# Kernel tuning notes

Measured on AMD Instinct MI355X. Metric: run time of the kernel, lower is better.

The kernel has to match this reference:

```python
import jax, jax.numpy as jnp
import numpy as np

N, E, C, L, G, O = 100000, 1600000, 128, 7, 2, 40
BETA = 0.9
HEADS, HC = 1, 128  # heads=1, head_channels=hidden_channels=128


def setup_inputs() -> dict:
    key = jax.random.key(0)
    ks = jax.random.split(key, 16)
    s = 0.05  # ~ torch Linear init std for fan_in=128
    inp = {
        'x': jax.random.normal(ks[0], (N, C), jnp.float32),
        'edge_index': jax.random.randint(ks[1], (2, E), 0, N, jnp.int64),
        'Wh': jax.random.normal(ks[2], (L, C, C)) * s,
        'bh': jax.random.normal(ks[3], (L, C)) * s,
        'Wg': jax.random.normal(ks[4], (L, C, C)) * s,
        'bg': jax.random.normal(ks[5], (L, C)) * s,
        'Wl': jax.random.normal(ks[6], (L, C, C)) * s,
        'bl': jax.random.normal(ks[7], (L, C)) * s,
        'ln_g': jnp.ones((L, C)), 'ln_b': jnp.zeros((L, C)),
        'bn_g': jnp.ones((L, C)), 'bn_b': jnp.zeros((L, C)),
        'bn_rm': jnp.zeros((L, C)), 'bn_rv': jnp.ones((L, C)),
        'gWh': jax.random.normal(ks[8], (G, C, C)) * s,
        'gbh': jax.random.normal(ks[9], (G, C)) * s,
        'gWk': jax.random.normal(ks[10], (G, C, C)) * s,
        'gWv': jax.random.normal(ks[11], (G, C, C)) * s,
        'gln_g': jnp.ones((G, C)), 'gln_b': jnp.zeros((G, C)),
        'gWo': jax.random.normal(ks[12], (G, C, C)) * s,
        'gbo': jax.random.normal(ks[13], (G, C)) * s,
        'f_ln_g': jnp.ones((C,)), 'f_ln_b': jnp.zeros((C,)),
        'Wp': jax.random.normal(ks[14], (O, C)) * s,
        'bp': jax.random.normal(ks[15], (O,)) * s,
    }
    return inp


def _layer_norm(x, g, b, eps=1e-5):
    mu = jnp.mean(x, axis=-1, keepdims=True)
    var = jnp.mean((x - mu) ** 2, axis=-1, keepdims=True)
    return (x - mu) * jax.lax.rsqrt(var + eps) * g + b


def reference(x, edge_index, Wh, bh, Wg, bg, Wl, bl, ln_g, ln_b,
              bn_g, bn_b, bn_rm, bn_rv, gWh, gbh, gWk, gWv,
              gln_g, gln_b, gWo, gbo, f_ln_g, f_ln_b, Wp, bp):
    n = x.shape[0]
    src, dst = edge_index[0], edge_index[1]
    # gcn_norm with add_self_loops=True: deg over destination incl. self loop
    deg = jnp.zeros((n,), x.dtype).at[dst].add(1.0) + 1.0
    dinv = jax.lax.rsqrt(deg)
    enorm = (dinv[src] * dinv[dst])[:, None]   # [E,1]
    selfw = (dinv * dinv)[:, None]             # [N,1] self-loop weight

    x_local = jnp.zeros_like(x @ Wh[0].T)
    for i in range(L):
        h = jax.nn.relu(x @ Wh[i].T + bh[i])
        xw = x @ Wg[i].T                                  # GCN lin (bias separate)
        agg = jax.ops.segment_sum(xw[src] * enorm, dst, num_segments=n)
        conv = agg + xw * selfw + bg[i]
        x = conv + x @ Wl[i].T + bl[i]
        # BatchNorm1d in eval mode (running stats)
        x = (x - bn_rm[i]) * jax.lax.rsqrt(bn_rv[i] + 1e-5) * bn_g[i] + bn_b[i]
        x = jax.nn.relu(x)
        x = (1.0 - BETA) * _layer_norm(h * x, ln_g[i], ln_b[i]) + BETA * x
        x_local = x_local + x

    # global linear attention (PolynormerAttention, qk_shared=True, qkv_bias=False)
    xg = _layer_norm(x_local, f_ln_g, f_ln_b)
    for j in range(G):
        h = xg @ gWh[j].T + gbh[j]
        k = jax.nn.sigmoid(xg @ gWk[j].T).reshape(n, HEADS, HC)
        q = k
        v = (xg @ gWv[j].T).reshape(n, HEADS, HC)
        kv = jnp.einsum('ndh,ndm->dhm', k, v)            # [heads,hc,hc]
        num = jnp.einsum('ndh,dhm->ndm', q, kv)          # [N,heads,hc]
        k_sum = jnp.sum(k, axis=0)                       # [heads,hc]
        den = jnp.einsum('ndh,dh->nd', q, k_sum)[..., None]
        attn = (num / (den + 1e-6)).reshape(n, HEADS * HC)
        xg = _layer_norm(attn, gln_g[j], gln_b[j]) * (h + BETA)
        xg = jax.nn.relu(xg @ gWo[j].T + gbo[j])

    return xg @ Wp.T + bp
```

## Files before the change

### kernel.cpp

```cpp
#include <hip/hip_runtime.h>

typedef unsigned short u16;
typedef unsigned int u32;
typedef __attribute__((ext_vector_type(8))) short short8;
typedef __attribute__((ext_vector_type(8))) unsigned short ushort8v;
typedef __attribute__((ext_vector_type(4))) float f32x4;

#define CDIM 128

__device__ __forceinline__ float b2f(u16 u){ return __uint_as_float(((unsigned)u)<<16); }
__device__ __forceinline__ u16 f2b(float f){
  unsigned x = __float_as_uint(f);
  unsigned r = (x + 0x7fffu + ((x>>16)&1u)) >> 16;
  return (u16)r;
}
__device__ __forceinline__ float wsum64(float v){
  #pragma unroll
  for(int d=1; d<64; d<<=1) v += __shfl_xor(v, d, 64);
  return v;
}
__device__ __forceinline__ float wsum16(float v){
  v += __shfl_xor(v, 1, 64);
  v += __shfl_xor(v, 2, 64);
  v += __shfl_xor(v, 4, 64);
  v += __shfl_xor(v, 8, 64);
  return v;
}

__global__ void k_probe(const u32* __restrict__ x, const u32* __restrict__ ei, int* __restrict__ flags){
  __shared__ int s_bf, s_nz;
  if(threadIdx.x == 0){ s_bf = 0; s_nz = 0; }
  __syncthreads();
  int c_bf = 0, c_nz = 0;
  for(int i = threadIdx.x; i < 4096; i += 256){
    u32 w = x[i];
    u32 e = (w >> 7) & 0xFFu;
    if(e >= 100u && e <= 140u) c_bf++;
    if(ei[2*i + 1] != 0u) c_nz++;
  }
  atomicAdd(&s_bf, c_bf);
  atomicAdd(&s_nz, c_nz);
  __syncthreads();
  if(threadIdx.x == 0){
    flags[0] = (s_bf < 2048) ? 1 : 0;
    flags[1] = (s_nz < 8) ? 1 : 0;
  }
}

__global__ void k_cvt_x(const void* __restrict__ src, u16* __restrict__ dst, int n,
                        const int* __restrict__ flags){
  int i = (blockIdx.x*256 + threadIdx.x)*8;
  if(i + 7 >= n) return;
  if(flags[0]){
    const float* s = (const float*)src + i;
    float4 a = *(const float4*)s;
    float4 b = *(const float4*)(s + 4);
    ushort8v o;
    o[0]=f2b(a.x); o[1]=f2b(a.y); o[2]=f2b(a.z); o[3]=f2b(a.w);
    o[4]=f2b(b.x); o[5]=f2b(b.y); o[6]=f2b(b.z); o[7]=f2b(b.w);
    *(ushort8v*)(dst + i) = o;
  } else {
    *(ushort8v*)(dst + i) = *(const ushort8v*)((const u16*)src + i);
  }
}

struct CvtArgs {
  const void* src[24];
  u16* dst[24];
  int n[24];
};

__global__ void k_cvt_params(CvtArgs a, const int* __restrict__ flags){
  int seg = blockIdx.y;
  int i = blockIdx.x*256 + threadIdx.x;
  int n = a.n[seg];
  if(i >= n) return;
  if(flags[0]) a.dst[seg][i] = f2b(((const float*)a.src[seg])[i]);
  else         a.dst[seg][i] = ((const u16*)a.src[seg])[i];
}

__global__ void k_cvt_ei_count(const int* __restrict__ src, int* __restrict__ dst, int E,
                               const int* __restrict__ flags, u32* __restrict__ cnt){
  int i = blockIdx.x*256 + threadIdx.x;
  if(i >= 2*E) return;
  int v = flags[1] ? src[2*i] : src[i];
  dst[i] = v;
  if(i >= E) atomicAdd(&cnt[v], 1u);
}

__global__ __launch_bounds__(256) void k_scan1(const u32* __restrict__ cnt, int n, u32* __restrict__ bsum){
  const int lane = threadIdx.x & 63;
  const int wv = threadIdx.x >> 6;
  int i = blockIdx.x*256 + threadIdx.x;
  u32 v = (i < n) ? cnt[i] : 0u;
  #pragma unroll
  for(int d=1; d<64; d<<=1) v += (u32)__shfl_xor((int)v, d, 64);
  __shared__ u32 ws[4];
  if(lane == 0) ws[wv] = v;
  __syncthreads();
  if(threadIdx.x == 0) bsum[blockIdx.x] = ws[0] + ws[1] + ws[2] + ws[3];
}

__global__ __launch_bounds__(1024) void k_scan2(const u32* __restrict__ bsum, int nb, u32* __restrict__ bpre){
  __shared__ u32 s[1024];
  int t = threadIdx.x;
  u32 v = (t < nb) ? bsum[t] : 0u;
  s[t] = v;
  __syncthreads();
  for(int d=1; d<1024; d<<=1){
    u32 y = (t >= d) ? s[t-d] : 0u;
    __syncthreads();
    s[t] += y;
    __syncthreads();
  }
  if(t < nb) bpre[t] = s[t] - v;
}

__global__ __launch_bounds__(256) void k_scan3(const u32* __restrict__ cnt, int n,
                                               const u32* __restrict__ bpre,
                                               u32* __restrict__ rowstart, u32* __restrict__ cursor,
                                               float* __restrict__ dinv){
  const int lane = threadIdx.x & 63;
  const int wv = threadIdx.x >> 6;
  int i = blockIdx.x*256 + threadIdx.x;
  u32 v = (i < n) ? cnt[i] : 0u;
  u32 x = v;
  #pragma unroll
  for(int d=1; d<64; d<<=1){
    u32 y = (u32)__shfl_up((int)x, d, 64);
    if(lane >= d) x += y;
  }
  __shared__ u32 ws[4];
  if(lane == 63) ws[wv] = x;
  __syncthreads();
  u32 woff = 0;
  #pragma unroll
  for(int w=0; w<4; w++) if(w < wv) woff += ws[w];
  u32 incl = x + woff;
  u32 rs = bpre[blockIdx.x] + incl - v;
  if(i < n){
    rowstart[i] = rs;
    cursor[i] = rs;
    dinv[i] = rsqrtf((float)(v + 1u));
    if(i == n-1) rowstart[n] = rs + v;
  }
}

__global__ __launch_bounds__(256) void k_scatter8(
  const int* __restrict__ ei, int E, int Nn, int nsl,
  u32* __restrict__ cursor, const float* __restrict__ dinv, int2* __restrict__ colw)
{
  const int r = blockIdx.x & 7;
  const int slice = blockIdx.x >> 3;
  const int q = (Nn + 7) >> 3;
  const int lo = r*q;
  const int hi = (lo + q < Nn) ? lo + q : Nn;
  const int chunk = (E + nsl - 1) / nsl;
  int e0 = slice*chunk;
  int e1 = e0 + chunk; if(e1 > E) e1 = E;
  for(int e = e0 + threadIdx.x; e < e1; e += 256){
    int d = ei[E + e];
    if(d >= lo && d < hi){
      int s = ei[e];
      u32 p = atomicAdd(&cursor[d], 1u);
      colw[p] = make_int2(s, __float_as_int(dinv[s]));
    }
  }
}

__global__ __launch_bounds__(256) void k_gemm3(
  const u16* __restrict__ A, int M,
  const u16* __restrict__ W0, const u16* __restrict__ bs0, int op0, u16* __restrict__ O0,
  const u16* __restrict__ W1, const u16* __restrict__ bs1, int op1, u16* __restrict__ O1,
  const u16* __restrict__ W2, const u16* __restrict__ bs2, int op2, u16* __restrict__ O2)
{
  __shared__ u16 stg[4][64][72];
  const int lane = threadIdx.x & 63;
  const int wv = threadIdx.x >> 6;
  const int l16 = lane & 15, quad = lane >> 4;
  const long nbase = (long)blockIdx.x*256 + wv*64;
  u16 (*st)[72] = stg[wv];

  const int w = blockIdx.y;
  const u16* Wm = (w==0) ? W0 : (w==1) ? W1 : W2;
  const u16* bp = (w==0) ? bs0 : (w==1) ? bs1 : bs2;
  const int  op = (w==0) ? op0 : (w==1) ? op1 : op2;
  u16*       Op = (w==0) ? O0 : (w==1) ? O1 : O2;

  short8 xf[4][4];
  #pragma unroll
  for(int nt=0; nt<4; nt++){
    long r = nbase + nt*16 + l16; if(r >= M) r = M-1;
    const u16* ap = A + r*CDIM + quad*8;
    #pragma unroll
    for(int kt=0; kt<4; kt++)
      xf[nt][kt] = *(const short8*)(ap + kt*32);
  }

  const int srow = lane >> 3;
  const int schk = lane & 7;

  #pragma unroll
  for(int half=0; half<2; half++){
    #pragma unroll
    for(int c2=0; c2<4; c2++){
      const int ct = half*4 + c2;
      f32x4 acc[4];
      #pragma unroll
      for(int nt=0; nt<4; nt++) acc[nt] = (f32x4){0.f,0.f,0.f,0.f};
      const u16* wp = Wm + (ct*16 + l16)*CDIM + quad*8;
      #pragma unroll
      for(int kt=0; kt<4; kt++){
        short8 wf = *(const short8*)(wp + kt*32);
        #pragma unroll
        for(int nt=0; nt<4; nt++)
          acc[nt] = __builtin_amdgcn_mfma_f32_16x16x32_bf16(wf, xf[nt][kt], acc[nt], 0, 0, 0);
      }
      float bv[4] = {0.f,0.f,0.f,0.f};
      if(bp){
        ushort4 bq = *(const ushort4*)(bp + ct*16 + quad*4);
        bv[0]=b2f(bq.x); bv[1]=b2f(bq.y); bv[2]=b2f(bq.z); bv[3]=b2f(bq.w);
      }
      #pragma unroll
      for(int nt=0; nt<4; nt++){
        u16 o[4];
        #pragma unroll
        for(int g=0; g<4; g++){
          float v = acc[nt][g] + bv[g];
          if(op == 1) v = fmaxf(v, 0.f);
          else if(op == 2) v = 1.f/(1.f + __expf(-v));
          o[g] = f2b(v);
        }
        u32 p0 = (u32)o[0] | ((u32)o[1] << 16);
        u32 p1 = (u32)o[2] | ((u32)o[3] << 16);
        *(uint2*)&st[nt*16 + l16][c2*16 + quad*4] = make_uint2(p0, p1);
      }
    }
    #pragma unroll
    for(int i=0; i<8; i++){
      int row = i*8 + srow;
      long node = nbase + row;
      ushort8v v = *(const ushort8v*)&st[row][schk*8];
      if(node < M)
        *(ushort8v*)(Op + (size_t)node*CDIM + half*64 + schk*8) = v;
    }
  }
}

__global__ __launch_bounds__(256) void k_layer_epi(
  const u16* __restrict__ xw, const u16* __restrict__ h, const u16* __restrict__ xl,
  const int2* __restrict__ colw, const u32* __restrict__ rowstart, const float* __restrict__ dinv,
  const u16* __restrict__ bg, const u16* __restrict__ bng, const u16* __restrict__ bnb,
  const u16* __restrict__ bnrm, const u16* __restrict__ bnrv,
  const u16* __restrict__ lng, const u16* __restrict__ lnb,
  const u16* __restrict__ flng, const u16* __restrict__ flnb,
  float* __restrict__ xlocal, u16* __restrict__ xout, int n, int first, int final)
{
  const int lane = threadIdx.x & 63;
  const int quad = lane >> 4;
  const int l16 = lane & 15;
  const int wv = threadIdx.x >> 6;
  int node = blockIdx.x*16 + wv*4 + quad;
  const int valid = (node < n);
  if(!valid) node = n - 1;
  const int cg = l16*8;
  u32 j0 = rowstart[node], j1 = rowstart[node+1];
  float a[8];
  #pragma unroll
  for(int g=0; g<8; g++) a[g] = 0.f;

  for(u32 base = j0; base < j1; base += 16){
    int cnt = (int)(j1 - base); if(cnt > 16) cnt = 16;
    int2 pw = make_int2(0, 0);
    if(l16 < cnt) pw = colw[base + l16];
    ushort8v v[16]; float w[16];
    #pragma unroll
    for(int u=0; u<16; u++){
      int s = __shfl(pw.x, quad*16 + u, 64);
      w[u] = __int_as_float(__shfl(pw.y, quad*16 + u, 64));
      v[u] = *(const ushort8v*)(xw + (size_t)s*CDIM + cg);
    }
    #pragma unroll
    for(int u=0; u<16; u++){
      #pragma unroll
      for(int g=0; g<8; g++) a[g] = fmaf(w[u], b2f(v[u][g]), a[g]);
    }
  }

  float dn = dinv[node], sw = dn*dn;
  size_t nb = (size_t)node*CDIM + cg;
  ushort8v xwv  = *(const ushort8v*)(xw + nb);
  ushort8v xlv  = *(const ushort8v*)(xl + nb);
  ushort8v hv   = *(const ushort8v*)(h  + nb);
  ushort8v bgv  = *(const ushort8v*)(bg + cg);
  ushort8v bngv = *(const ushort8v*)(bng + cg);
  ushort8v bnbv = *(const ushort8v*)(bnb + cg);
  ushort8v bnrmv= *(const ushort8v*)(bnrm + cg);
  ushort8v bnrvv= *(const ushort8v*)(bnrv + cg);
  ushort8v lngv = *(const ushort8v*)(lng + cg);
  ushort8v lnbv = *(const ushort8v*)(lnb + cg);

  float x3[8], t[8];
  float ts = 0.f;
  #pragma unroll
  for(int g=0; g<8; g++){
    float x1 = a[g]*dn + b2f(xwv[g])*sw + b2f(bgv[g]) + b2f(xlv[g]);
    float sc = rsqrtf(b2f(bnrvv[g]) + 1e-5f) * b2f(bngv[g]);
    float x2 = (x1 - b2f(bnrmv[g]))*sc + b2f(bnbv[g]);
    x3[g] = fmaxf(x2, 0.f);
    t[g] = b2f(hv[g]) * x3[g];
    ts += t[g];
  }
  float mu = wsum16(ts) * (1.f/128.f);
  float vs = 0.f;
  #pragma unroll
  for(int g=0; g<8; g++){ float d = t[g] - mu; vs = fmaf(d, d, vs); }
  float inv = rsqrtf(wsum16(vs)*(1.f/128.f) + 1e-5f);

  float xn[8], xl2[8];
  #pragma unroll
  for(int g=0; g<8; g++){
    float y = (t[g] - mu)*inv*b2f(lngv[g]) + b2f(lnbv[g]);
    xn[g] = 0.1f*y + 0.9f*x3[g];
  }
  if(first){
    #pragma unroll
    for(int g=0; g<8; g++) xl2[g] = xn[g];
  } else {
    f32x4 p0 = *(const f32x4*)(xlocal + nb);
    f32x4 p1 = *(const f32x4*)(xlocal + nb + 4);
    xl2[0]=p0[0]+xn[0]; xl2[1]=p0[1]+xn[1]; xl2[2]=p0[2]+xn[2]; xl2[3]=p0[3]+xn[3];
    xl2[4]=p1[0]+xn[4]; xl2[5]=p1[1]+xn[5]; xl2[6]=p1[2]+xn[6]; xl2[7]=p1[3]+xn[7];
  }
  if(!final){
    if(valid){
      f32x4 q0 = {xl2[0],xl2[1],xl2[2],xl2[3]};
      f32x4 q1 = {xl2[4],xl2[5],xl2[6],xl2[7]};
      *(f32x4*)(xlocal + nb)     = q0;
      *(f32x4*)(xlocal + nb + 4) = q1;
      ushort8v o;
      #pragma unroll
      for(int g=0; g<8; g++) o[g] = f2b(xn[g]);
      *(ushort8v*)(xout + nb) = o;
    }
  } else {
    float ss = 0.f;
    #pragma unroll
    for(int g=0; g<8; g++) ss += xl2[g];
    float mu2 = wsum16(ss) * (1.f/128.f);
    float v2 = 0.f;
    #pragma unroll
    for(int g=0; g<8; g++){ float e = xl2[g] - mu2; v2 = fmaf(e, e, v2); }
    float inv2 = rsqrtf(wsum16(v2)*(1.f/128.f) + 1e-5f);
    ushort8v flngv = *(const ushort8v*)(flng + cg);
    ushort8v flnbv = *(const ushort8v*)(flnb + cg);
    if(valid){
      ushort8v o;
      #pragma unroll
      for(int g=0; g<8; g++)
        o[g] = f2b((xl2[g] - mu2)*inv2*b2f(flngv[g]) + b2f(flnbv[g]));
      *(ushort8v*)(xout + nb) = o;
    }
  }
}

__global__ __launch_bounds__(256) void k_kv(
  const u16* __restrict__ kk, const u16* __restrict__ vv, int n, int npb,
  float* __restrict__ part)
{
  __shared__ float sk[8][128];
  __shared__ float sv[8][128];
  const int tid = threadIdx.x;
  const int tr = tid >> 4, tc = tid & 15;
  float acc[8][8];
  #pragma unroll
  for(int i=0;i<8;i++){
    #pragma unroll
    for(int j=0;j<8;j++) acc[i][j] = 0.f;
  }
  float ks[8];
  #pragma unroll
  for(int i=0;i<8;i++) ks[i] = 0.f;
  int start = blockIdx.x * npb;
  int end = start + npb; if(end > n) end = n;
  const int lr = tid >> 5;
  const int lc = (tid & 31) * 4;
  for(int g0 = start; g0 < end; g0 += 8){
    int cnt = end - g0; if(cnt > 8) cnt = 8;
    __syncthreads();
    if(lr < cnt){
      ushort4 kq = *(const ushort4*)(kk + (size_t)(g0+lr)*CDIM + lc);
      ushort4 vq = *(const ushort4*)(vv + (size_t)(g0+lr)*CDIM + lc);
      sk[lr][lc] = b2f(kq.x); sk[lr][lc+1] = b2f(kq.y); sk[lr][lc+2] = b2f(kq.z); sk[lr][lc+3] = b2f(kq.w);
      sv[lr][lc] = b2f(vq.x); sv[lr][lc+1] = b2f(vq.y); sv[lr][lc+2] = b2f(vq.z); sv[lr][lc+3] = b2f(vq.w);
    }
    __syncthreads();
    for(int r=0; r<cnt; r++){
      float4 ka = *(const float4*)&sk[r][tr*8];
      float4 kb = *(const float4*)&sk[r][tr*8+4];
      float4 va = *(const float4*)&sv[r][tc*8];
      float4 vb = *(const float4*)&sv[r][tc*8+4];
      float kr[8] = {ka.x,ka.y,ka.z,ka.w,kb.x,kb.y,kb.z,kb.w};
      float vr[8] = {va.x,va.y,va.z,va.w,vb.x,vb.y,vb.z,vb.w};
      #pragma unroll
      for(int i=0;i<8;i++){
        #pragma unroll
        for(int j=0;j<8;j++) acc[i][j] = fmaf(kr[i], vr[j], acc[i][j]);
      }
      if(tc == 0){
        #pragma unroll
        for(int i=0;i<8;i++) ks[i] += kr[i];
      }
    }
  }
  float* p = part + (size_t)blockIdx.x * 16512;
  #pragma unroll
  for(int i=0;i<8;i++){
    #pragma unroll
    for(int j=0;j<8;j++)
      p[(size_t)(tc*8+j)*CDIM + tr*8 + i] = acc[i][j];
  }
  if(tc == 0){
    #pragma unroll
    for(int i=0;i<8;i++) p[16384 + tr*8 + i] = ks[i];
  }
}

__global__ void k_kvred(const float* __restrict__ part, int nb, u16* __restrict__ Bext){
  int i = blockIdx.x*256 + threadIdx.x;
  if(i >= 144*128) return;
  float s = 0.f;
  if(i < 16512){
    #pragma unroll 8
    for(int b=0;b<nb;b++) s += part[(size_t)b*16512 + i];
  }
  Bext[i] = f2b(s);
}

__global__ __launch_bounds__(256) void k_attn(
  const u16* __restrict__ q, const u16* __restrict__ Bext, const u16* __restrict__ hg,
  const u16* __restrict__ g, const u16* __restrict__ b,
  const u16* __restrict__ Wo, const u16* __restrict__ bo,
  const u16* __restrict__ Wp, const u16* __restrict__ bp,
  u16* __restrict__ xgout, void* __restrict__ outv,
  int M, int last, const int* __restrict__ flags)
{
  __shared__ u16 stg[4][32*136];
  const int lane = threadIdx.x & 63;
  const int wv = threadIdx.x >> 6;
  const int l16 = lane & 15, quad = lane >> 4;
  const long rbase = (long)blockIdx.x*128 + wv*32;
  u16* st = stg[wv];

  {
    short8 af[2][4];
    #pragma unroll
    for(int rt=0; rt<2; rt++){
      long r = rbase + rt*16 + l16; if(r >= M) r = M-1;
      const u16* ap = q + r*CDIM + quad*8;
      #pragma unroll
      for(int kt=0; kt<4; kt++)
        af[rt][kt] = *(const short8*)(ap + kt*32);
    }
    f32x4 acc[2][9];
    f32x4 zero = {0.f,0.f,0.f,0.f};
    #pragma unroll
    for(int rt=0; rt<2; rt++){
      #pragma unroll
      for(int ct=0; ct<9; ct++) acc[rt][ct] = zero;
    }
    #pragma unroll
    for(int ct=0; ct<9; ct++){
      const u16* wp = Bext + (ct*16 + l16)*CDIM + quad*8;
      #pragma unroll
      for(int kt=0; kt<4; kt++){
        short8 bf = *(const short8*)(wp + kt*32);
        acc[0][ct] = __builtin_amdgcn_mfma_f32_16x16x32_bf16(af[0][kt], bf, acc[0][ct], 0, 0, 0);
        acc[1][ct] = __builtin_amdgcn_mfma_f32_16x16x32_bf16(af[1][kt], bf, acc[1][ct], 0, 0, 0);
      }
    }
    #pragma unroll
    for(int rt=0; rt<2; rt++){
      float rden[4];
      #pragma unroll
      for(int gi=0; gi<4; gi++){
        float dv = __shfl(acc[rt][8][gi], lane & 48, 64);
        rden[gi] = 1.f/(dv + 1e-6f);
      }
      #pragma unroll
      for(int gi=0; gi<4; gi++){
        float sum = 0.f;
        #pragma unroll
        for(int ct=0; ct<8; ct++) sum += acc[rt][ct][gi]*rden[gi];
        float mu = wsum16(sum) * (1.f/128.f);
        float vs = 0.f;
        #pragma unroll
        for(int ct=0; ct<8; ct++){ float d = acc[rt][ct][gi]*rden[gi] - mu; vs = fmaf(d, d, vs); }
        float inv = rsqrtf(wsum16(vs)*(1.f/128.f) + 1e-5f);
        const int rowl = rt*16 + quad*4 + gi;
        #pragma unroll
        for(int ct=0; ct<8; ct++){
          int col = ct*16 + l16;
          float y = (acc[rt][ct][gi]*rden[gi] - mu)*inv*b2f(g[col]) + b2f(b[col]);
          st[rowl*136 + col] = f2b(y);
        }
      }
    }
  }
  #pragma unroll
  for(int p2=0; p2<8; p2++){
    int row = (p2>>2)*16 + (lane>>2);
    int seg = (lane&3) + (p2&3)*4;
    long node = rbase + row;
    if(node >= M) node = M-1;
    ushort8v yv = *(const ushort8v*)&st[row*136 + seg*8];
    ushort8v hv = *(const ushort8v*)(hg + (size_t)node*CDIM + seg*8);
    ushort8v o;
    #pragma unroll
    for(int i2=0; i2<8; i2++)
      o[i2] = f2b(b2f(yv[i2]) * (b2f(hv[i2]) + 0.9f));
    *(ushort8v*)&st[row*136 + seg*8] = o;
  }
  short8 pf[2][4];
  #pragma unroll
  for(int nt=0; nt<2; nt++){
    #pragma unroll
    for(int kt=0; kt<4; kt++)
      pf[nt][kt] = *(const short8*)&st[(nt*16 + l16)*136 + quad*8 + kt*32];
  }
  #pragma unroll
  for(int ct=0; ct<8; ct++){
    f32x4 a0 = {0.f,0.f,0.f,0.f}, a1 = {0.f,0.f,0.f,0.f};
    const u16* wp = Wo + (ct*16 + l16)*CDIM + quad*8;
    #pragma unroll
    for(int kt=0; kt<4; kt++){
      short8 wf = *(const short8*)(wp + kt*32);
      a0 = __builtin_amdgcn_mfma_f32_16x16x32_bf16(wf, pf[0][kt], a0, 0, 0, 0);
      a1 = __builtin_amdgcn_mfma_f32_16x16x32_bf16(wf, pf[1][kt], a1, 0, 0, 0);
    }
    ushort4 bq = *(const ushort4*)(bo + ct*16 + quad*4);
    float bv[4] = {b2f(bq.x), b2f(bq.y), b2f(bq.z), b2f(bq.w)};
    #pragma unroll
    for(int nt=0; nt<2; nt++){
      f32x4 a = nt ? a1 : a0;
      u16 o[4];
      #pragma unroll
      for(int g2=0; g2<4; g2++)
        o[g2] = f2b(fmaxf(a[g2] + bv[g2], 0.f));
      u32 p0 = (u32)o[0] | ((u32)o[1] << 16);
      u32 p1 = (u32)o[2] | ((u32)o[3] << 16);
      *(uint2*)&st[(nt*16 + l16)*136 + ct*16 + quad*4] = make_uint2(p0, p1);
    }
  }
  if(!last){
    #pragma unroll
    for(int p2=0; p2<8; p2++){
      int row = (p2>>2)*16 + (lane>>2);
      int seg = (lane&3) + (p2&3)*4;
      long node = rbase + row;
      ushort8v v = *(const ushort8v*)&st[row*136 + seg*8];
      if(node < M)
        *(ushort8v*)(xgout + (size_t)node*CDIM + seg*8) = v;
    }
  } else {
    const int f32m = flags[0];
    short8 pf2[2][4];
    #pragma unroll
    for(int nt=0; nt<2; nt++){
      #pragma unroll
      for(int kt=0; kt<4; kt++)
        pf2[nt][kt] = *(const short8*)&st[(nt*16 + l16)*136 + quad*8 + kt*32];
    }
    #pragma unroll
    for(int ct=0; ct<3; ct++){
      f32x4 a0 = {0.f,0.f,0.f,0.f}, a1 = {0.f,0.f,0.f,0.f};
      int wrow = ct*16 + l16; if(wrow > 39) wrow = 39;
      const u16* wp = Wp + wrow*CDIM + quad*8;
      #pragma unroll
      for(int kt=0; kt<4; kt++){
        short8 wf = *(const short8*)(wp + kt*32);
        a0 = __builtin_amdgcn_mfma_f32_16x16x32_bf16(wf, pf2[0][kt], a0, 0, 0, 0);
        a1 = __builtin_amdgcn_mfma_f32_16x16x32_bf16(wf, pf2[1][kt], a1, 0, 0, 0);
      }
      const int ch0 = ct*16 + quad*4;
      if(ch0 < 40){
        ushort4 bq = *(const ushort4*)(bp + ch0);
        float bv[4] = {b2f(bq.x), b2f(bq.y), b2f(bq.z), b2f(bq.w)};
        #pragma unroll
        for(int nt=0; nt<2; nt++){
          long node = rbase + nt*16 + l16;
          if(node < M){
            f32x4 a = nt ? a1 : a0;
            if(f32m){
              float* op = (float*)outv + node*40 + ch0;
              #pragma unroll
              for(int g2=0; g2<4; g2++) op[g2] = a[g2] + bv[g2];
            } else {
              u16 o[4];
              #pragma unroll
              for(int g2=0; g2<4; g2++) o[g2] = f2b(a[g2] + bv[g2]);
              u32 p0 = (u32)o[0] | ((u32)o[1] << 16);
              u32 p1 = (u32)o[2] | ((u32)o[3] << 16);
              *(uint2*)((u16*)outv + node*40 + ch0) = make_uint2(p0, p1);
            }
          }
        }
      }
    }
  }
}

extern "C" void kernel_launch(void* const* d_in, const int* in_sizes, int n_in,
                              void* d_out, int out_size, void* d_ws, size_t ws_size,
                              hipStream_t stream)
{
  (void)n_in;
  const int C = CDIM;
  const int Nn = in_sizes[0] / C;
  const int E  = in_sizes[1] / 2;

  char* ws = (char*)d_ws;
  size_t off = 0;
  auto alloc = [&](size_t bytes) -> char* {
    char* p = ws + off;
    off = (off + bytes + 255) & ~(size_t)255;
    return p;
  };
  u16*   x_cur  = (u16*)  alloc((size_t)Nn*C*2);
  float* xlocal = (float*)alloc((size_t)Nn*C*4);
  u16*   hb     = (u16*)  alloc((size_t)Nn*C*2);
  u16*   xwb    = (u16*)  alloc((size_t)Nn*C*2);
  u16*   xlb    = (u16*)  alloc((size_t)Nn*C*2);
  float* dinv   = (float*)alloc((size_t)Nn*4);
  u32*   cnt    = (u32*)  alloc((size_t)Nn*4);
  u32*   rowst  = (u32*)  alloc((size_t)(Nn+1)*4);
  u32*   cursor = (u32*)  alloc((size_t)Nn*4);
  int2*  colw   = (int2*) alloc((size_t)E*8);
  u16*   Bext   = (u16*)  alloc((size_t)144*128*2);
  int*   flags  = (int*)  alloc(256);
  u32*   bsum   = (u32*)  alloc(1024*4);
  u32*   bpre   = (u32*)  alloc(1024*4);
  size_t ptot = 0;
  for(int k=2;k<26;k++) ptot += (size_t)in_sizes[k];
  u16* pbuf = (u16*)alloc(ptot*2);

  if(off > ws_size){
    hipMemsetAsync(d_out, 0, (size_t)out_size*2, stream);
    return;
  }

  const u16* pp[26];
  {
    size_t po = 0;
    for(int k=2;k<26;k++){ pp[k] = pbuf + po; po += (size_t)in_sizes[k]; }
  }
  const u16* cWh  = pp[2];  const u16* cbh  = pp[3];
  const u16* cWg  = pp[4];  const u16* cbg  = pp[5];
  const u16* cWl  = pp[6];  const u16* cbl  = pp[7];
  const u16* clng = pp[8];  const u16* clnb = pp[9];
  const u16* cbng = pp[10]; const u16* cbnb = pp[11];
  const u16* cbnrm= pp[12]; const u16* cbnrv= pp[13];
  const u16* cgWh = pp[14]; const u16* cgbh = pp[15];
  const u16* cgWk = pp[16]; const u16* cgWv = pp[17];
  const u16* cglng= pp[18]; const u16* cglnb= pp[19];
  const u16* cgWo = pp[20]; const u16* cgbo = pp[21];
  const u16* cflng= pp[22]; const u16* cflnb= pp[23];
  const u16* cWp  = pp[24]; const u16* cbp  = pp[25];

  u16* xb  = (u16*)xlocal;
  int* eib = (int*)((char*)xlocal + (size_t)Nn*C*2);
  u16* xg  = x_cur;
  float* kvpart = xlocal;

  const int NB_KV = 512;
  const int npb = (Nn + NB_KV - 1) / NB_KV;
  const int gblk = (Nn + 127) / 128;
  const int gblk4 = (Nn + 255) / 256;
  const int nodeblk = (Nn + 15) / 16;
  const int nscan = (Nn + 255) / 256;
  const int NSL = 512;

  k_probe<<<1, 256, 0, stream>>>((const u32*)d_in[0], (const u32*)d_in[1], flags);
  hipMemsetAsync(cnt, 0, (size_t)Nn*4, stream);
  k_cvt_ei_count<<<(2*E + 255)/256, 256, 0, stream>>>((const int*)d_in[1], eib, E, flags, cnt);
  k_cvt_x<<<(Nn*C/8 + 255)/256, 256, 0, stream>>>(d_in[0], xb, Nn*C, flags);
  {
    CvtArgs a;
    int maxn = 0;
    for(int k=2;k<26;k++){
      a.src[k-2] = d_in[k];
      a.dst[k-2] = (u16*)pp[k];
      a.n[k-2]   = in_sizes[k];
      if(in_sizes[k] > maxn) maxn = in_sizes[k];
    }
    dim3 g((maxn + 255)/256, 24);
    k_cvt_params<<<g, 256, 0, stream>>>(a, flags);
  }

  k_scan1<<<nscan, 256, 0, stream>>>(cnt, Nn, bsum);
  k_scan2<<<1, 1024, 0, stream>>>(bsum, nscan, bpre);
  k_scan3<<<nscan, 256, 0, stream>>>(cnt, Nn, bpre, rowst, cursor, dinv);
  k_scatter8<<<NSL*8, 256, 0, stream>>>(eib, E, Nn, NSL, cursor, dinv, colw);

  const u16* xa = xb;
  for(int i=0; i<7; i++){
    k_gemm3<<<dim3(gblk4,3), 256, 0, stream>>>(xa, Nn,
        cWh + (size_t)i*C*C, cbh + (size_t)i*C, 1, hb,
        cWg + (size_t)i*C*C, (const u16*)nullptr, 0, xwb,
        cWl + (size_t)i*C*C, cbl + (size_t)i*C, 0, xlb);
    k_layer_epi<<<nodeblk, 256, 0, stream>>>(xwb, hb, xlb, colw, rowst, dinv,
        cbg + (size_t)i*C, cbng + (size_t)i*C, cbnb + (size_t)i*C,
        cbnrm + (size_t)i*C, cbnrv + (size_t)i*C,
        clng + (size_t)i*C, clnb + (size_t)i*C,
        cflng, cflnb,
        xlocal, x_cur, Nn, (i==0) ? 1 : 0, (i==6) ? 1 : 0);
    xa = x_cur;
  }

  for(int j=0; j<2; j++){
    k_gemm3<<<dim3(gblk4,3), 256, 0, stream>>>(xg, Nn,
        cgWh + (size_t)j*C*C, cgbh + (size_t)j*C, 0, hb,
        cgWk + (size_t)j*C*C, (const u16*)nullptr, 2, xwb,
        cgWv + (size_t)j*C*C, (const u16*)nullptr, 0, xlb);
    k_kv   <<<NB_KV, 256, 0, stream>>>(xwb, xlb, Nn, npb, kvpart);
    k_kvred<<<(144*128 + 255)/256, 256, 0, stream>>>(kvpart, NB_KV, Bext);
    k_attn <<<gblk, 256, 0, stream>>>(xwb, Bext, hb,
        cglng + (size_t)j*C, cglnb + (size_t)j*C,
        cgWo + (size_t)j*C*C, cgbo + (size_t)j*C,
        cWp, cbp, xg, d_out, Nn, (j==1) ? 1 : 0, flags);
  }
}
```

Before: 1.618 ms.

## Fuse the h and linear-skip GEMMs into the layer epilogue kernel

The per-layer GEMM now computes only the GCN projection xw. The h (relu) and linear-skip projections are computed inside k_layer_epi with MFMA for each 16-node block and staged in shared memory. This removes the global write and re-read of the hb and xlb intermediates on every layer. In exchange, every epilogue block re-reads both 128x128 weight matrices (mostly from cache) and does small 16-row MFMA tiles. The initial bf16 x buffer is moved into hb so it no longer aliases xlocal, which the epilogue writes.

```diff
diff --git a/kernel.cpp b/kernel.cpp
--- a/kernel.cpp
+++ b/kernel.cpp
@@ -248,7 +248,9 @@
 }
 
 __global__ __launch_bounds__(256) void k_layer_epi(
-  const u16* __restrict__ xw, const u16* __restrict__ h, const u16* __restrict__ xl,
+  const u16* __restrict__ xa, const u16* __restrict__ xw,
+  const u16* __restrict__ Wh, const u16* __restrict__ bhp,
+  const u16* __restrict__ Wl, const u16* __restrict__ blp,
   const int2* __restrict__ colw, const u32* __restrict__ rowstart, const float* __restrict__ dinv,
   const u16* __restrict__ bg, const u16* __restrict__ bng, const u16* __restrict__ bnb,
   const u16* __restrict__ bnrm, const u16* __restrict__ bnrv,
@@ -256,11 +258,51 @@
   const u16* __restrict__ flng, const u16* __restrict__ flnb,
   float* __restrict__ xlocal, u16* __restrict__ xout, int n, int first, int final)
 {
+  __shared__ u16 sh_h[16][136];
+  __shared__ u16 sh_x[16][136];
   const int lane = threadIdx.x & 63;
   const int quad = lane >> 4;
   const int l16 = lane & 15;
   const int wv = threadIdx.x >> 6;
-  int node = blockIdx.x*16 + wv*4 + quad;
+  const long blk0 = (long)blockIdx.x*16;
+
+  {
+    long r = blk0 + l16; if(r >= n) r = n-1;
+    const u16* ap = xa + r*CDIM + quad*8;
+    short8 xf[4];
+    #pragma unroll
+    for(int kt=0; kt<4; kt++) xf[kt] = *(const short8*)(ap + kt*32);
+    #pragma unroll
+    for(int c2=0; c2<2; c2++){
+      const int ct = wv*2 + c2;
+      const u16* wph = Wh + (ct*16 + l16)*CDIM + quad*8;
+      const u16* wpl = Wl + (ct*16 + l16)*CDIM + quad*8;
+      f32x4 ah = {0.f,0.f,0.f,0.f}, al = {0.f,0.f,0.f,0.f};
+      #pragma unroll
+      for(int kt=0; kt<4; kt++){
+        short8 wfh = *(const short8*)(wph + kt*32);
+        short8 wfl = *(const short8*)(wpl + kt*32);
+        ah = __builtin_amdgcn_mfma_f32_16x16x32_bf16(wfh, xf[kt], ah, 0, 0, 0);
+        al = __builtin_amdgcn_mfma_f32_16x16x32_bf16(wfl, xf[kt], al, 0, 0, 0);
+      }
+      ushort4 bhq = *(const ushort4*)(bhp + ct*16 + quad*4);
+      ushort4 blq = *(const ushort4*)(blp + ct*16 + quad*4);
+      float bhv[4] = {b2f(bhq.x), b2f(bhq.y), b2f(bhq.z), b2f(bhq.w)};
+      float blv[4] = {b2f(blq.x), b2f(blq.y), b2f(blq.z), b2f(blq.w)};
+      u16 oh[4], ol[4];
+      #pragma unroll
+      for(int g=0; g<4; g++){
+        oh[g] = f2b(fmaxf(ah[g] + bhv[g], 0.f));
+        ol[g] = f2b(al[g] + blv[g]);
+      }
+      *(uint2*)&sh_h[l16][ct*16 + quad*4] = make_uint2((u32)oh[0] | ((u32)oh[1]<<16), (u32)oh[2] | ((u32)oh[3]<<16));
+      *(uint2*)&sh_x[l16][ct*16 + quad*4] = make_uint2((u32)ol[0] | ((u32)ol[1]<<16), (u32)ol[2] | ((u32)ol[3]<<16));
+    }
+  }
+  __syncthreads();
+
+  const int slot = wv*4 + quad;
+  int node = blockIdx.x*16 + slot;
   const int valid = (node < n);
   if(!valid) node = n - 1;
   const int cg = l16*8;
@@ -290,8 +332,8 @@
   float dn = dinv[node], sw = dn*dn;
   size_t nb = (size_t)node*CDIM + cg;
   ushort8v xwv  = *(const ushort8v*)(xw + nb);
-  ushort8v xlv  = *(const ushort8v*)(xl + nb);
-  ushort8v hv   = *(const ushort8v*)(h  + nb);
+  ushort8v xlv  = *(const ushort8v*)&sh_x[slot][cg];
+  ushort8v hv   = *(const ushort8v*)&sh_h[slot][cg];
   ushort8v bgv  = *(const ushort8v*)(bg + cg);
   ushort8v bngv = *(const ushort8v*)(bng + cg);
   ushort8v bnbv = *(const ushort8v*)(bnb + cg);
@@ -667,7 +709,7 @@
   const u16* cflng= pp[22]; const u16* cflnb= pp[23];
   const u16* cWp  = pp[24]; const u16* cbp  = pp[25];
 
-  u16* xb  = (u16*)xlocal;
+  u16* xb  = hb;
   int* eib = (int*)((char*)xlocal + (size_t)Nn*C*2);
   u16* xg  = x_cur;
   float* kvpart = xlocal;
@@ -704,11 +746,14 @@
 
   const u16* xa = xb;
   for(int i=0; i<7; i++){
-    k_gemm3<<<dim3(gblk4,3), 256, 0, stream>>>(xa, Nn,
-        cWh + (size_t)i*C*C, cbh + (size_t)i*C, 1, hb,
+    k_gemm3<<<dim3(gblk4,1), 256, 0, stream>>>(xa, Nn,
         cWg + (size_t)i*C*C, (const u16*)nullptr, 0, xwb,
-        cWl + (size_t)i*C*C, cbl + (size_t)i*C, 0, xlb);
-    k_layer_epi<<<nodeblk, 256, 0, stream>>>(xwb, hb, xlb, colw, rowst, dinv,
+        (const u16*)nullptr, (const u16*)nullptr, 0, (u16*)nullptr,
+        (const u16*)nullptr, (const u16*)nullptr, 0, (u16*)nullptr);
+    k_layer_epi<<<nodeblk, 256, 0, stream>>>(xa, xwb,
+        cWh + (size_t)i*C*C, cbh + (size_t)i*C,
+        cWl + (size_t)i*C*C, cbl + (size_t)i*C,
+        colw, rowst, dinv,
         cbg + (size_t)i*C, cbng + (size_t)i*C, cbnb + (size_t)i*C,
         cbnrm + (size_t)i*C, cbnrv + (size_t)i*C,
         clng + (size_t)i*C, clnb + (size_t)i*C,
```

New measurement: 1.679 ms. 1.04x slower.
